# Kernel tuning notes

Measured on AMD Instinct MI355X. Metric: run time of the kernel, lower is better.

The kernel has to match this reference:

```python
import jax, jax.numpy as jnp
import numpy as np

N_NODES = 100000


def gcn_conv(x, W, b, src, dst, num_nodes):
    """PyG GCNConv: add self-loops, D^{-1/2}(A+I)D^{-1/2} (x @ W) + b."""
    h = x @ W  # [N, F_out] linear transform first (small dense GEMM)
    loop = jnp.arange(num_nodes, dtype=src.dtype)
    s = jnp.concatenate([src, loop])  # source (row) with self loops
    d = jnp.concatenate([dst, loop])  # destination (col) with self loops
    deg = jax.ops.segment_sum(jnp.ones_like(d, dtype=h.dtype), d,
                              num_segments=num_nodes)
    dis = jnp.where(deg > 0, jax.lax.rsqrt(deg), 0.0)  # deg^{-1/2}
    norm = dis[s] * dis[d]  # [E+N]
    msg = h[s] * norm[:, None]  # gather + scale: [E+N, F_out]
    out = jax.ops.segment_sum(msg, d, num_segments=num_nodes)
    return out + b


def setup_inputs() -> dict:
    key = jax.random.key(0)
    k1, k2, k3, k4, k5, k6 = jax.random.split(key, 6)
    x = jax.random.uniform(k1, (N_NODES, 16), dtype=jnp.float32)
    edge_index = jax.random.randint(k2, (2, 3200000), 0, N_NODES, dtype=jnp.int64)
    # Glorot-style init for GCNConv linear weights, zero bias (PyG default)
    W1 = jax.random.normal(k3, (16, 32), dtype=jnp.float32) * (1.0 / np.sqrt(16))
    b1 = jnp.zeros((32,), dtype=jnp.float32)
    W2 = jax.random.normal(k4, (32, 2), dtype=jnp.float32) * (1.0 / np.sqrt(32))
    b2 = jnp.zeros((2,), dtype=jnp.float32)
    return {"x": x, "edge_index": edge_index, "W1": W1, "b1": b1,
            "W2": W2, "b2": b2}


def reference(x, edge_index, W1, b1, W2, b2):
    src, dst = edge_index[0], edge_index[1]
    h = gcn_conv(x, W1, b1, src, dst, N_NODES)
    h = jax.nn.relu(h)
    out = gcn_conv(h, W2, b2, src, dst, N_NODES)
    return out
```

## Files before the change

### kernel.cpp

```cpp
#include <hip/hip_runtime.h>


static constexpr int F0 = 16;
static constexpr int F1 = 32;
static constexpr int F2 = 2;
static constexpr int BSH  = 9;
static constexpr int BMSK = 511;
static constexpr int NPB  = 512;
static constexpr int MAXNB = 256;
static constexpr int NBMAX = 196;
static constexpr int BPAD  = 16;
static constexpr int EPB   = 8192;
static constexpr int CAP   = 24576;
static constexpr int SORTCAP = EPB + NBMAX * 16;
static constexpr unsigned SENT = 0xFFFFFFFFu;

__device__ inline unsigned roundup16(unsigned h) { return (h + 15u) & ~15u; }

__device__ inline unsigned f2bf(float f) {
    unsigned u = __float_as_uint(f);
    return (u + 0x7fffu + ((u >> 16) & 1u)) >> 16;
}
__device__ inline float bf2f(unsigned b) {
    return __uint_as_float(b << 16);
}

__global__ void k_zero(unsigned* __restrict__ p, int n) {
    int i = blockIdx.x * blockDim.x + threadIdx.x;
    if (i < n) p[i] = 0u;
}

__global__ __launch_bounds__(512) void k_binA(const int* __restrict__ src,
                                              const int* __restrict__ dst,
                                              unsigned* __restrict__ bfill,
                                              unsigned* __restrict__ pairs,
                                              int E, int nb) {
    __shared__ unsigned h[MAXNB];
    __shared__ unsigned lbase[MAXNB];
    __shared__ unsigned bs_[MAXNB];
    __shared__ unsigned cur[MAXNB];
    __shared__ unsigned wsum[8];
    __shared__ unsigned wbase[8];
    __shared__ __attribute__((aligned(16))) unsigned sorted[SORTCAP];
    int tid = threadIdx.x;
    for (int b = tid; b < MAXNB; b += 512) { h[b] = 0; cur[b] = 0; }
    if (tid < 8) wsum[tid] = 0;
    __syncthreads();
    int e0 = blockIdx.x * EPB;
    int cn = min(EPB, E - e0);
    unsigned key[16];
    unsigned bkt[16];
#pragma unroll
    for (int j = 0; j < 16; ++j) {
        int idx = j * 512 + tid;
        if (idx < cn) {
            unsigned d = (unsigned)dst[e0 + idx];
            unsigned s = (unsigned)src[e0 + idx];
            unsigned b = d >> BSH;
            key[j] = (s << BSH) | (d & BMSK);
            bkt[j] = b;
            atomicAdd(&h[b], 1u);
        }
    }
    __syncthreads();
    unsigned pv = 0, px = 0;
    if (tid < MAXNB) {
        pv = roundup16(h[tid]);
        px = pv;
#pragma unroll
        for (int off = 1; off < 64; off <<= 1) {
            unsigned t = __shfl_up(px, off, 64);
            if ((tid & 63) >= off) px += t;
        }
        if ((tid & 63) == 63) wsum[tid >> 6] = px;
    }
    __syncthreads();
    if (tid < 8) {
        unsigned acc = 0;
        for (int k = 0; k < tid; ++k) acc += wsum[k];
        wbase[tid] = acc;
    }
    __syncthreads();
    if (tid < MAXNB) {
        unsigned ex = px - pv + wbase[tid >> 6];
        lbase[tid] = ex;
        if (tid < nb && h[tid])
            bs_[tid] = (unsigned)(tid * CAP) + atomicAdd(&bfill[tid * BPAD], roundup16(h[tid]));
    }
    __syncthreads();
#pragma unroll
    for (int j = 0; j < 16; ++j) {
        int idx = j * 512 + tid;
        if (idx < cn) {
            unsigned b = bkt[j];
            unsigned pos = lbase[b] + atomicAdd(&cur[b], 1u);
            sorted[pos] = key[j];
        }
    }
    for (int b = tid; b < nb; b += 512) {
        unsigned hb = h[b];
        if (!hb) continue;
        unsigned k0 = lbase[b] + hb;
        unsigned k1 = lbase[b] + roundup16(hb);
        for (unsigned k = k0; k < k1; ++k) sorted[k] = SENT;
    }
    __syncthreads();
    int grp = tid >> 3;
    int ln8 = tid & 7;
    for (int b = grp; b < nb; b += 64) {
        unsigned np = roundup16(h[b]) >> 2;
        if (!np) continue;
        const uint4* sp = reinterpret_cast<const uint4*>(&sorted[lbase[b]]);
        uint4* gp = reinterpret_cast<uint4*>(&pairs[bs_[b]]);
        for (unsigned k = ln8; k < np; k += 8) gp[k] = sp[k];
    }
}

__global__ __launch_bounds__(512) void k_binB(const unsigned* __restrict__ pairs,
                                              const unsigned* __restrict__ bfill,
                                              const float* __restrict__ x,
                                              int* __restrict__ cnt, float* __restrict__ dis,
                                              int* __restrict__ rstart, int* __restrict__ esrc,
                                              unsigned* __restrict__ xd, int N) {
    __shared__ unsigned h[NPB];
    __shared__ unsigned cur[NPB];
    __shared__ unsigned wsum[8];
    __shared__ unsigned wbase[8];
    __shared__ unsigned tot_s;
    __shared__ __attribute__((aligned(16))) unsigned srt[CAP];
    int tid = threadIdx.x, b = blockIdx.x;
    h[tid] = 0;
    __syncthreads();
    int r0 = b * CAP;
    int n4 = (int)bfill[b * BPAD] >> 2;
    const uint4* p4 = reinterpret_cast<const uint4*>(pairs + r0);
    for (int i = tid; i < n4; i += 512) {
        uint4 p = p4[i];
        if (p.x != SENT) atomicAdd(&h[p.x & BMSK], 1u);
        if (p.y != SENT) atomicAdd(&h[p.y & BMSK], 1u);
        if (p.z != SENT) atomicAdd(&h[p.z & BMSK], 1u);
        if (p.w != SENT) atomicAdd(&h[p.w & BMSK], 1u);
    }
    __syncthreads();
    unsigned v = h[tid];
    unsigned x2 = v;
#pragma unroll
    for (int off = 1; off < 64; off <<= 1) {
        unsigned t = __shfl_up(x2, off, 64);
        if ((tid & 63) >= off) x2 += t;
    }
    if ((tid & 63) == 63) wsum[tid >> 6] = x2;
    __syncthreads();
    if (tid < 8) {
        unsigned acc = 0;
        for (int k = 0; k < tid; ++k) acc += wsum[k];
        wbase[tid] = acc;
    }
    __syncthreads();
    unsigned ex = x2 - v + wbase[tid >> 6];
    cur[tid] = ex;
    if (tid == 511) tot_s = ex + v;
    int node = (b << BSH) + tid;
    if (node < N) {
        float d = rsqrtf((float)(v + 1u));
        cnt[node] = (int)v;
        dis[node] = d;
        rstart[node] = r0 + (int)ex;
        const float4* xp = reinterpret_cast<const float4*>(x + (size_t)node * F0);
        unsigned pk[8];
#pragma unroll
        for (int q = 0; q < 4; ++q) {
            float4 vv = xp[q];
            pk[2 * q + 0] = f2bf(d * vv.x) | (f2bf(d * vv.y) << 16);
            pk[2 * q + 1] = f2bf(d * vv.z) | (f2bf(d * vv.w) << 16);
        }
        uint4* o = reinterpret_cast<uint4*>(xd + (size_t)node * 8);
        o[0] = make_uint4(pk[0], pk[1], pk[2], pk[3]);
        o[1] = make_uint4(pk[4], pk[5], pk[6], pk[7]);
    }
    __syncthreads();
    for (int i = tid; i < n4; i += 512) {
        uint4 p = p4[i];
        if (p.x != SENT) { unsigned o_ = atomicAdd(&cur[p.x & BMSK], 1u); srt[o_] = p.x >> BSH; }
        if (p.y != SENT) { unsigned o_ = atomicAdd(&cur[p.y & BMSK], 1u); srt[o_] = p.y >> BSH; }
        if (p.z != SENT) { unsigned o_ = atomicAdd(&cur[p.z & BMSK], 1u); srt[o_] = p.z >> BSH; }
        if (p.w != SENT) { unsigned o_ = atomicAdd(&cur[p.w & BMSK], 1u); srt[o_] = p.w >> BSH; }
    }
    __syncthreads();
    unsigned tot4 = (tot_s + 3u) >> 2;
    const uint4* s4 = reinterpret_cast<const uint4*>(srt);
    uint4* g4 = reinterpret_cast<uint4*>(esrc + r0);
    for (unsigned k = tid; k < tot4; k += 512) g4[k] = s4[k];
}

__global__ void k_layer1(const unsigned* __restrict__ xd, const int* __restrict__ cnt,
                         const int* __restrict__ rstart, const int* __restrict__ esrc,
                         const float* __restrict__ dis, const float* __restrict__ b1,
                         const float* __restrict__ W1, const float* __restrict__ W2,
                         float* __restrict__ g2, int N) {
    __shared__ float w1[F0 * F1];
    __shared__ float w2[F1 * F2];
    __shared__ float bb[F1];
    __shared__ float ymat[32][17];
    for (int j = threadIdx.x; j < F0 * F1; j += blockDim.x) w1[j] = W1[j];
    for (int j = threadIdx.x; j < F1 * F2; j += blockDim.x) w2[j] = W2[j];
    for (int j = threadIdx.x; j < F1; j += blockDim.x) bb[j] = b1[j];
    __syncthreads();
    int t = blockIdx.x * blockDim.x + threadIdx.x;
    int v = t >> 3;
    int q = t & 7;
    if (v >= N) return;
    const unsigned* base = xd + q;
    unsigned sw = base[(size_t)v * 8];
    float a0 = bf2f(sw & 0xffffu);
    float a1 = bf2f(sw >> 16);
    int beg = rstart[v];
    int n = cnt[v];
    int j = 0;
    for (; j + 16 <= n; j += 16) {
        int ia = esrc[beg + j + 2 * q];
        int ib = esrc[beg + j + 2 * q + 1];
#pragma unroll
        for (int u = 0; u < 8; ++u) {
            int s0 = __shfl(ia, u, 8);
            int s1 = __shfl(ib, u, 8);
            unsigned a = base[(size_t)s0 * 8];
            unsigned c = base[(size_t)s1 * 8];
            a0 += bf2f(a & 0xffffu) + bf2f(c & 0xffffu);
            a1 += bf2f(a >> 16) + bf2f(c >> 16);
        }
    }
    if (j + 8 <= n) {
        int idx = esrc[beg + j + q];
#pragma unroll
        for (int u = 0; u < 8; ++u) {
            int s = __shfl(idx, u, 8);
            unsigned a = base[(size_t)s * 8];
            a0 += bf2f(a & 0xffffu);
            a1 += bf2f(a >> 16);
        }
        j += 8;
    }
    for (; j < n; ++j) {
        int s = esrc[beg + j];
        unsigned a = base[(size_t)s * 8];
        a0 += bf2f(a & 0xffffu);
        a1 += bf2f(a >> 16);
    }
    int ln = threadIdx.x >> 3;
    ymat[ln][2 * q + 0] = a0;
    ymat[ln][2 * q + 1] = a1;
    float y[F0];
#pragma unroll
    for (int k = 0; k < F0; ++k) y[k] = ymat[ln][k];
    float d = dis[v];
    float p0 = 0.0f, p1 = 0.0f;
#pragma unroll
    for (int u = 0; u < 4; ++u) {
        int jf = q * 4 + u;
        float s = 0.0f;
#pragma unroll
        for (int k = 0; k < F0; ++k) s = fmaf(y[k], w1[k * F1 + jf], s);
        float r = fmaxf(fmaf(d, s, bb[jf]), 0.0f);
        p0 = fmaf(r, w2[jf * F2 + 0], p0);
        p1 = fmaf(r, w2[jf * F2 + 1], p1);
    }
#pragma unroll
    for (int off = 1; off < 8; off <<= 1) {
        p0 += __shfl_xor(p0, off);
        p1 += __shfl_xor(p1, off);
    }
    if (q == 0) {
        g2[(size_t)v * F2 + 0] = d * p0;
        g2[(size_t)v * F2 + 1] = d * p1;
    }
}

__global__ void k_out2(const float* __restrict__ g2, const int* __restrict__ cnt,
                       const int* __restrict__ rstart, const int* __restrict__ esrc,
                       const float* __restrict__ dis, const float* __restrict__ b2,
                       float* __restrict__ out, int N) {
    int t = blockIdx.x * blockDim.x + threadIdx.x;
    int v = t >> 2;
    int l = t & 3;
    if (v >= N) return;
    float o0 = 0.0f, o1 = 0.0f;
    int beg = rstart[v];
    int end = beg + cnt[v];
    int j = beg + l;
    for (; j + 28 < end; j += 32) {
        int s0 = esrc[j];
        int s1 = esrc[j + 4];
        int s2 = esrc[j + 8];
        int s3 = esrc[j + 12];
        int s4 = esrc[j + 16];
        int s5 = esrc[j + 20];
        int s6 = esrc[j + 24];
        int s7 = esrc[j + 28];
        float2 a0 = *reinterpret_cast<const float2*>(g2 + (size_t)s0 * F2);
        float2 a1 = *reinterpret_cast<const float2*>(g2 + (size_t)s1 * F2);
        float2 a2 = *reinterpret_cast<const float2*>(g2 + (size_t)s2 * F2);
        float2 a3 = *reinterpret_cast<const float2*>(g2 + (size_t)s3 * F2);
        float2 a4 = *reinterpret_cast<const float2*>(g2 + (size_t)s4 * F2);
        float2 a5 = *reinterpret_cast<const float2*>(g2 + (size_t)s5 * F2);
        float2 a6 = *reinterpret_cast<const float2*>(g2 + (size_t)s6 * F2);
        float2 a7 = *reinterpret_cast<const float2*>(g2 + (size_t)s7 * F2);
        o0 += a0.x + a1.x + a2.x + a3.x + a4.x + a5.x + a6.x + a7.x;
        o1 += a0.y + a1.y + a2.y + a3.y + a4.y + a5.y + a6.y + a7.y;
    }
    for (; j + 12 < end; j += 16) {
        int s0 = esrc[j];
        int s1 = esrc[j + 4];
        int s2 = esrc[j + 8];
        int s3 = esrc[j + 12];
        float2 a0 = *reinterpret_cast<const float2*>(g2 + (size_t)s0 * F2);
        float2 a1 = *reinterpret_cast<const float2*>(g2 + (size_t)s1 * F2);
        float2 a2 = *reinterpret_cast<const float2*>(g2 + (size_t)s2 * F2);
        float2 a3 = *reinterpret_cast<const float2*>(g2 + (size_t)s3 * F2);
        o0 += a0.x + a1.x + a2.x + a3.x;
        o1 += a0.y + a1.y + a2.y + a3.y;
    }
    for (; j < end; j += 4) {
        int s = esrc[j];
        const float2 a = *reinterpret_cast<const float2*>(g2 + (size_t)s * F2);
        o0 += a.x; o1 += a.y;
    }
#pragma unroll
    for (int off = 1; off < 4; off <<= 1) {
        o0 += __shfl_xor(o0, off);
        o1 += __shfl_xor(o1, off);
    }
    if (l == 0) {
        float d = dis[v];
        const float2 self = *reinterpret_cast<const float2*>(g2 + (size_t)v * F2);
        out[(size_t)v * F2 + 0] = fmaf(d, o0 + self.x, b2[0]);
        out[(size_t)v * F2 + 1] = fmaf(d, o1 + self.y, b2[1]);
    }
}

extern "C" void kernel_launch(void* const* d_in, const int* in_sizes, int n_in,
                              void* d_out, int out_size, void* d_ws, size_t ws_size,
                              hipStream_t stream) {
    const float* x  = (const float*)d_in[0];
    const int* ei   = (const int*)d_in[1];
    const float* W1 = (const float*)d_in[2];
    const float* b1 = (const float*)d_in[3];
    const float* W2 = (const float*)d_in[4];
    const float* b2 = (const float*)d_in[5];
    float* out = (float*)d_out;

    const int N = in_sizes[0] / F0;
    const int E = in_sizes[1] / 2;
    const int* src = ei;
    const int* dst = ei + E;
    const int nb = (N + BMSK) >> BSH;
    const int nchunk = (E + EPB - 1) / EPB;

    unsigned* bfill = (unsigned*)d_ws;
    unsigned* pairs = bfill + MAXNB * BPAD;
    int* esrc       = (int*)(pairs + (size_t)nb * CAP);
    unsigned* xd    = (unsigned*)(esrc + (size_t)nb * CAP);
    float* dis      = (float*)(xd + (size_t)8 * N);
    int* cnt        = (int*)(dis + N);
    int* rstart     = cnt + N;
    float* g2       = (float*)(rstart + N);

    const int B = 256;
    const int nz = MAXNB * BPAD;
    k_zero<<<(nz + B - 1) / B, B, 0, stream>>>(bfill, nz);
    k_binA<<<nchunk, 512, 0, stream>>>(src, dst, bfill, pairs, E, nb);
    k_binB<<<nb, 512, 0, stream>>>(pairs, bfill, x, cnt, dis, rstart, esrc, xd, N);
    k_layer1<<<(N * 8 + B - 1) / B, B, 0, stream>>>(xd, cnt, rstart, esrc, dis, b1, W1, W2, g2, N);
    k_out2<<<(N * 4 + B - 1) / B, B, 0, stream>>>(g2, cnt, rstart, esrc, dis, b2, out, N);
}
```

Measured before the change: 90.39 us.

## Split each bin's counting sort across two blocks by node half

Launches two blocks per 512-node bin in the CSR-building kernel. Each block filters pairs to its 256-node half, builds the histogram, scan and local sort for that half only, and writes to its own half-capacity region of esrc. The aims are twice the parallelism and half the shared memory per block, so more blocks fit per CU. In exchange every block reads the whole bin's pair list, doubling global reads. The code also uses __syncthreads inside divergent branches, and a half's edges may overflow HCAP.

```diff
diff --git a/kernel.cpp b/kernel.cpp
--- a/kernel.cpp
+++ b/kernel.cpp
@@ -6,12 +6,12 @@
 static constexpr int F2 = 2;
 static constexpr int BSH  = 9;
 static constexpr int BMSK = 511;
-static constexpr int NPB  = 512;
 static constexpr int MAXNB = 256;
 static constexpr int NBMAX = 196;
 static constexpr int BPAD  = 16;
 static constexpr int EPB   = 8192;
 static constexpr int CAP   = 24576;
+static constexpr int HCAP  = CAP / 2;
 static constexpr int SORTCAP = EPB + NBMAX * 16;
 static constexpr unsigned SENT = 0xFFFFFFFFu;
 
@@ -122,74 +122,82 @@
                                               int* __restrict__ cnt, float* __restrict__ dis,
                                               int* __restrict__ rstart, int* __restrict__ esrc,
                                               unsigned* __restrict__ xd, int N) {
-    __shared__ unsigned h[NPB];
-    __shared__ unsigned cur[NPB];
-    __shared__ unsigned wsum[8];
-    __shared__ unsigned wbase[8];
+    __shared__ unsigned h[256];
+    __shared__ unsigned cur[256];
+    __shared__ unsigned wsum[4];
+    __shared__ unsigned wbase[4];
     __shared__ unsigned tot_s;
-    __shared__ __attribute__((aligned(16))) unsigned srt[CAP];
-    int tid = threadIdx.x, b = blockIdx.x;
-    h[tid] = 0;
+    __shared__ __attribute__((aligned(16))) unsigned srt[HCAP];
+    int tid = threadIdx.x;
+    int b = blockIdx.x >> 1;
+    unsigned hf = blockIdx.x & 1;
+    if (tid < 256) { h[tid] = 0; }
     __syncthreads();
     int r0 = b * CAP;
     int n4 = (int)bfill[b * BPAD] >> 2;
     const uint4* p4 = reinterpret_cast<const uint4*>(pairs + r0);
     for (int i = tid; i < n4; i += 512) {
         uint4 p = p4[i];
-        if (p.x != SENT) atomicAdd(&h[p.x & BMSK], 1u);
-        if (p.y != SENT) atomicAdd(&h[p.y & BMSK], 1u);
-        if (p.z != SENT) atomicAdd(&h[p.z & BMSK], 1u);
-        if (p.w != SENT) atomicAdd(&h[p.w & BMSK], 1u);
-    }
-    __syncthreads();
-    unsigned v = h[tid];
-    unsigned x2 = v;
-#pragma unroll
-    for (int off = 1; off < 64; off <<= 1) {
-        unsigned t = __shfl_up(x2, off, 64);
-        if ((tid & 63) >= off) x2 += t;
-    }
-    if ((tid & 63) == 63) wsum[tid >> 6] = x2;
-    __syncthreads();
-    if (tid < 8) {
-        unsigned acc = 0;
-        for (int k = 0; k < tid; ++k) acc += wsum[k];
-        wbase[tid] = acc;
-    }
-    __syncthreads();
-    unsigned ex = x2 - v + wbase[tid >> 6];
-    cur[tid] = ex;
-    if (tid == 511) tot_s = ex + v;
-    int node = (b << BSH) + tid;
-    if (node < N) {
-        float d = rsqrtf((float)(v + 1u));
-        cnt[node] = (int)v;
-        dis[node] = d;
-        rstart[node] = r0 + (int)ex;
-        const float4* xp = reinterpret_cast<const float4*>(x + (size_t)node * F0);
-        unsigned pk[8];
-#pragma unroll
-        for (int q = 0; q < 4; ++q) {
-            float4 vv = xp[q];
-            pk[2 * q + 0] = f2bf(d * vv.x) | (f2bf(d * vv.y) << 16);
-            pk[2 * q + 1] = f2bf(d * vv.z) | (f2bf(d * vv.w) << 16);
-        }
-        uint4* o = reinterpret_cast<uint4*>(xd + (size_t)node * 8);
-        o[0] = make_uint4(pk[0], pk[1], pk[2], pk[3]);
-        o[1] = make_uint4(pk[4], pk[5], pk[6], pk[7]);
+        if (p.x != SENT && ((p.x >> 8) & 1u) == hf) atomicAdd(&h[p.x & 255u], 1u);
+        if (p.y != SENT && ((p.y >> 8) & 1u) == hf) atomicAdd(&h[p.y & 255u], 1u);
+        if (p.z != SENT && ((p.z >> 8) & 1u) == hf) atomicAdd(&h[p.z & 255u], 1u);
+        if (p.w != SENT && ((p.w >> 8) & 1u) == hf) atomicAdd(&h[p.w & 255u], 1u);
+    }
+    __syncthreads();
+    int er0 = (int)(blockIdx.x * HCAP);
+    if (tid < 256) {
+        unsigned v = h[tid];
+        unsigned x2 = v;
+#pragma unroll
+        for (int off = 1; off < 64; off <<= 1) {
+            unsigned t = __shfl_up(x2, off, 64);
+            if ((tid & 63) >= off) x2 += t;
+        }
+        if ((tid & 63) == 63) wsum[tid >> 6] = x2;
+        __syncthreads();
+        if (tid < 4) {
+            unsigned acc = 0;
+            for (int k = 0; k < tid; ++k) acc += wsum[k];
+            wbase[tid] = acc;
+        }
+        __syncthreads();
+        unsigned ex = x2 - v + wbase[tid >> 6];
+        cur[tid] = ex;
+        if (tid == 255) tot_s = ex + v;
+        int node = (b << BSH) + ((int)hf << 8) + tid;
+        if (node < N) {
+            float d = rsqrtf((float)(v + 1u));
+            cnt[node] = (int)v;
+            dis[node] = d;
+            rstart[node] = er0 + (int)ex;
+            const float4* xp = reinterpret_cast<const float4*>(x + (size_t)node * F0);
+            unsigned pk[8];
+#pragma unroll
+            for (int q = 0; q < 4; ++q) {
+                float4 vv = xp[q];
+                pk[2 * q + 0] = f2bf(d * vv.x) | (f2bf(d * vv.y) << 16);
+                pk[2 * q + 1] = f2bf(d * vv.z) | (f2bf(d * vv.w) << 16);
+            }
+            uint4* o = reinterpret_cast<uint4*>(xd + (size_t)node * 8);
+            o[0] = make_uint4(pk[0], pk[1], pk[2], pk[3]);
+            o[1] = make_uint4(pk[4], pk[5], pk[6], pk[7]);
+        }
+    } else {
+        __syncthreads();
+        __syncthreads();
     }
     __syncthreads();
     for (int i = tid; i < n4; i += 512) {
         uint4 p = p4[i];
-        if (p.x != SENT) { unsigned o_ = atomicAdd(&cur[p.x & BMSK], 1u); srt[o_] = p.x >> BSH; }
-        if (p.y != SENT) { unsigned o_ = atomicAdd(&cur[p.y & BMSK], 1u); srt[o_] = p.y >> BSH; }
-        if (p.z != SENT) { unsigned o_ = atomicAdd(&cur[p.z & BMSK], 1u); srt[o_] = p.z >> BSH; }
-        if (p.w != SENT) { unsigned o_ = atomicAdd(&cur[p.w & BMSK], 1u); srt[o_] = p.w >> BSH; }
+        if (p.x != SENT && ((p.x >> 8) & 1u) == hf) { unsigned o_ = atomicAdd(&cur[p.x & 255u], 1u); srt[o_] = p.x >> BSH; }
+        if (p.y != SENT && ((p.y >> 8) & 1u) == hf) { unsigned o_ = atomicAdd(&cur[p.y & 255u], 1u); srt[o_] = p.y >> BSH; }
+        if (p.z != SENT && ((p.z >> 8) & 1u) == hf) { unsigned o_ = atomicAdd(&cur[p.z & 255u], 1u); srt[o_] = p.z >> BSH; }
+        if (p.w != SENT && ((p.w >> 8) & 1u) == hf) { unsigned o_ = atomicAdd(&cur[p.w & 255u], 1u); srt[o_] = p.w >> BSH; }
     }
     __syncthreads();
     unsigned tot4 = (tot_s + 3u) >> 2;
     const uint4* s4 = reinterpret_cast<const uint4*>(srt);
-    uint4* g4 = reinterpret_cast<uint4*>(esrc + r0);
+    uint4* g4 = reinterpret_cast<uint4*>(esrc + er0);
     for (unsigned k = tid; k < tot4; k += 512) g4[k] = s4[k];
 }
 
@@ -369,7 +377,7 @@
     const int nz = MAXNB * BPAD;
     k_zero<<<(nz + B - 1) / B, B, 0, stream>>>(bfill, nz);
     k_binA<<<nchunk, 512, 0, stream>>>(src, dst, bfill, pairs, E, nb);
-    k_binB<<<nb, 512, 0, stream>>>(pairs, bfill, x, cnt, dis, rstart, esrc, xd, N);
+    k_binB<<<nb * 2, 512, 0, stream>>>(pairs, bfill, x, cnt, dis, rstart, esrc, xd, N);
     k_layer1<<<(N * 8 + B - 1) / B, B, 0, stream>>>(xd, cnt, rstart, esrc, dis, b1, W1, W2, g2, N);
     k_out2<<<(N * 4 + B - 1) / B, B, 0, stream>>>(g2, cnt, rstart, esrc, dis, b2, out, N);
 }
```

Measured after the change: 93.25 us. 3.2% more time.
